# Optimization experiments

Hardware: AMD Instinct MI355X
Metric: run time of the kernel (lower is better)

Reference implementation:

```python
import jax, jax.numpy as jnp
import numpy as np

DT = 0.01


def setup_inputs() -> dict:
    key = jax.random.key(0)
    ks = jax.random.split(key, 16)
    B, T, IN, S, N, OUT, H = 512, 2048, 32, 16, 128, 8, 64
    sc = 0.1
    return {
        "obs": jax.random.normal(ks[0], (B, T, IN), jnp.float32),
        "x0": jnp.zeros((B, S), jnp.float32),
        "A_T": sc * jax.random.normal(ks[1], (S, S), jnp.float32),
        "Bw_T": sc * jax.random.normal(ks[2], (N, S), jnp.float32),
        "By_T": sc * jax.random.normal(ks[3], (IN, S), jnp.float32),
        "Cv_T": sc * jax.random.normal(ks[4], (S, N), jnp.float32),
        "Dvy_T": sc * jax.random.normal(ks[5], (IN, N), jnp.float32),
        "Cu_T": sc * jax.random.normal(ks[6], (S, OUT), jnp.float32),
        "Duw_T": sc * jax.random.normal(ks[7], (N, OUT), jnp.float32),
        "Duy_T": sc * jax.random.normal(ks[8], (IN, OUT), jnp.float32),
        "log_stds": jnp.full((OUT,), -1.6094379124341003, jnp.float32),
        "W1": sc * jax.random.normal(ks[9], (IN, H), jnp.float32),
        "b1": jnp.zeros((H,), jnp.float32),
        "W2": sc * jax.random.normal(ks[10], (H, H), jnp.float32),
        "b2": jnp.zeros((H,), jnp.float32),
        "W3": sc * jax.random.normal(ks[11], (H, 1), jnp.float32),
        "b3": jnp.zeros((1,), jnp.float32),
    }


def reference(obs, x0, A_T, Bw_T, By_T, Cv_T, Dvy_T, Cu_T, Duw_T, Duy_T,
              log_stds, W1, b1, W2, b2, W3, b3):
    B, T, _ = obs.shape

    def xdot(x, y, w=None):
        if w is None:
            w = jnp.tanh(x @ Cv_T + y @ Dvy_T)
        return x @ A_T + w @ Bw_T + y @ By_T

    def step(x, y):
        # y: [B, IN], x: [B, S]
        w = jnp.tanh(x @ Cv_T + y @ Dvy_T)          # [B, N]
        u = x @ Cu_T + w @ Duw_T + y @ Duy_T        # [B, OUT]
        k1 = xdot(x, y, w=w)
        k2 = xdot(x + DT * k1 / 2, y)
        k3 = xdot(x + DT * k2 / 2, y)
        k4 = xdot(x + DT * k3, y)
        x_next = x + DT / 6 * (k1 + 2 * k2 + 2 * k3 + k4)
        return x_next, u

    obs_t = jnp.swapaxes(obs, 0, 1)                 # [T, B, IN]
    x_final, actions_t = jax.lax.scan(step, x0, obs_t)
    actions = jnp.swapaxes(actions_t, 0, 1)         # [B, T, OUT]

    log_stds_rep = jnp.broadcast_to(log_stds, actions.shape[:2] + log_stds.shape)
    outputs = jnp.concatenate((actions, log_stds_rep), axis=2)

    # value baseline MLP over raw observations
    h = jnp.tanh(obs @ W1 + b1)
    h = jnp.tanh(h @ W2 + b2)
    value = (h @ W3 + b3).reshape(-1)               # [B*T]
    return outputs, x_final, value
```

## Files before the change

kernel.cpp:

```cpp
#include <hip/hip_runtime.h>


#define B_SZ  512
#define T_LEN 2048
#define IN_D  32
#define S_D   16
#define N_D   128
#define OUT_D 8
#define H_D   64
#define DT_C  0.01f
#define CHUNK 8
#define NCH   (T_LEN / CHUNK)

typedef unsigned short u16;
typedef unsigned int   u32;
typedef unsigned int uv2 __attribute__((ext_vector_type(2)));

__device__ __forceinline__ float bf2f(u16 u){ return __uint_as_float(((u32)u)<<16); }
__device__ __forceinline__ float lo2f(u32 w){ return __uint_as_float(w<<16); }
__device__ __forceinline__ float hi2f(u32 w){ return __uint_as_float(w & 0xffff0000u); }
__device__ __forceinline__ u16 f2bf(float f){
    u32 u = __float_as_uint(f);
    u32 r = (u + 0x7fffu + ((u>>16)&1u)) >> 16;
    return (u16)r;
}
__device__ __forceinline__ float fast_tanh(float a){
    float e = __builtin_amdgcn_exp2f(a * 2.8853900817779268f);
    float r = __builtin_amdgcn_rcpf(e + 1.0f);
    return fmaf(-2.0f, r, 1.0f);
}
__device__ __forceinline__ u32 getc(const uint4& v, int c){
    return c==0 ? v.x : c==1 ? v.y : c==2 ? v.z : v.w;
}

#define QUAD1 0xB1
#define QUAD2 0x4E
#define QUAD3 0x1B
#define ROR8  0x128
#define HMIR  0x141
#define RMIR  0x140
template<int CTRL>
__device__ __forceinline__ float dppf(float v){
    return __int_as_float(__builtin_amdgcn_update_dpp(
        __float_as_int(v), __float_as_int(v), CTRL, 0xF, 0xF, false));
}
__device__ __forceinline__ float pl16sum(float v){
    uv2 r = __builtin_amdgcn_permlane16_swap(__float_as_uint(v), __float_as_uint(v), false, false);
    return __uint_as_float(r[0]) + __uint_as_float(r[1]);
}
__device__ __forceinline__ float pl32sum(float v){
    uv2 r = __builtin_amdgcn_permlane32_swap(__float_as_uint(v), __float_as_uint(v), false, false);
    return __uint_as_float(r[0]) + __uint_as_float(r[1]);
}

__device__ __forceinline__ int sig4(int d){ return (d&3) ^ ((d&4)?7:0) ^ (d&8); }
__device__ __forceinline__ int sig3(int d){ return (d&3) ^ ((d&4)?7:0); }

template<bool BF16>
__device__ __forceinline__ float ldw(const void* p, int i){
    if (BF16) return bf2f(((const u16*)p)[i]);
    else      return ((const float*)p)[i];
}
template<bool BF16>
__device__ __forceinline__ float yelem(const uint4* yr, int j){
    if (BF16) { u32 w = getc(yr[j>>3], (j>>1)&3); return (j&1) ? hi2f(w) : lo2f(w); }
    else      { return __uint_as_float(getc(yr[j>>2], j&3)); }
}
template<bool BF16>
__device__ __forceinline__ void ldrow(uint4* r, const void* obs, size_t row){
    const uint4* p = (const uint4*)((const char*)obs + row * (size_t)(IN_D * (BF16 ? 2 : 4)));
    #pragma unroll
    for (int q = 0; q < (BF16 ? 4 : 8); ++q) r[q] = p[q];
}
template<bool BF16>
__device__ __forceinline__ void stout(void* out, size_t i, float v){
    if (BF16) ((u16*)out)[i] = f2bf(v);
    else      ((float*)out)[i] = v;
}

template<bool BF16>
__global__ __attribute__((amdgpu_waves_per_eu(1, 1))) __launch_bounds__(128)
void rnn_fused(const void* __restrict__ obs,  const void* __restrict__ x0,
               const void* __restrict__ A_T,  const void* __restrict__ Bw_T,
               const void* __restrict__ By_T, const void* __restrict__ Cv_T,
               const void* __restrict__ Dvy_T,const void* __restrict__ Cu_T,
               const void* __restrict__ Duw_T,const void* __restrict__ Duy_T,
               const void* __restrict__ log_stds,
               const void* __restrict__ W1, const void* __restrict__ b1,
               const void* __restrict__ W2, const void* __restrict__ b2,
               const void* __restrict__ W3, const void* __restrict__ b3,
               void* __restrict__ out)
{
    {
        u32 w0 = *(const u32*)log_stds;
        bool is_bf16 = ((w0 & 0xffffu) == 0xBFCEu);
        if (is_bf16 != BF16) return;
    }

    const int b = blockIdx.x;
    const int t = threadIdx.x;
    const int l = t & 63;
    constexpr int NW = BF16 ? 4 : 8;

    __shared__ __align__(16) float yds[2][CHUNK][160];
    __shared__ __align__(16) float vh[2][64];

    const size_t XF_OFF  = (size_t)B_SZ * T_LEN * 16;
    const size_t VAL_OFF = XF_OFF + (size_t)B_SZ * S_D;

    if (t < 64) {
        const int cx = l & 15;
        const int o8 = l & 7;
        const int n0 = l, n1 = l + 64;

        float Cv0x[16], Cv1x[16], AxCol[16], CuCol[16];
        #pragma unroll
        for (int m = 0; m < 16; ++m) {
            int s = cx ^ m;
            Cv0x[m] = ldw<BF16>(Cv_T, s * N_D + n0);
            Cv1x[m] = ldw<BF16>(Cv_T, s * N_D + n1);
            AxCol[m] = ldw<BF16>(A_T,  s * S_D + cx);
            CuCol[m] = ldw<BF16>(Cu_T, s * OUT_D + o8);
        }
        float Bw0x[16], Bw1x[16];
        #pragma unroll
        for (int d = 0; d < 16; ++d) {
            int s = cx ^ sig4(d);
            Bw0x[d] = ldw<BF16>(Bw_T, n0 * S_D + s);
            Bw1x[d] = ldw<BF16>(Bw_T, n1 * S_D + s);
        }
        float Duw0x[8], Duw1x[8];
        #pragma unroll
        for (int d = 0; d < 8; ++d) {
            int o = o8 ^ sig3(d);
            Duw0x[d] = ldw<BF16>(Duw_T, n0 * OUT_D + o);
            Duw1x[d] = ldw<BF16>(Duw_T, n1 * OUT_D + o);
        }
        const float lsv = ldw<BF16>(log_stds, o8);

        float xb = ldw<BF16>(x0, b * S_D + cx);
        float g[16];
        #pragma unroll
        for (int m = 0; m < 16; ++m) g[m] = ldw<BF16>(x0, b * S_D + (cx ^ m));

        __syncthreads();

        for (int r = 0; r < NCH; ++r) {
            const float (*yb)[160] = yds[r & 1];
            float nD0 = yb[0][l];
            float nD1 = yb[0][64 + l];
            float nXv = yb[0][128 + cx];
            float nUv = yb[0][144 + o8];

            for (int j = 0; j < CHUNK; ++j) {
                const float yD0 = nD0, yD1 = nD1, yXv = nXv, yUv = nUv;
                if (j + 1 < CHUNK) {
                    nD0 = yb[j+1][l];
                    nD1 = yb[j+1][64 + l];
                    nXv = yb[j+1][128 + cx];
                    nUv = yb[j+1][144 + o8];
                }
                const int step = r * CHUNK + j;

                float kacc = 0.f;
                #pragma unroll
                for (int i = 0; i < 4; ++i) {
                    float a0a = 0.f, a0b = 0.f, a0c = 0.f, a0d = 0.f;
                    float a1a = 0.f, a1b = 0.f, a1c = 0.f, a1d = 0.f;
                    #pragma unroll
                    for (int m = 0; m < 4; ++m) {
                        a0a = fmaf(g[m],    Cv0x[m],    a0a);
                        a0b = fmaf(g[m+4],  Cv0x[m+4],  a0b);
                        a0c = fmaf(g[m+8],  Cv0x[m+8],  a0c);
                        a0d = fmaf(g[m+12], Cv0x[m+12], a0d);
                        a1a = fmaf(g[m],    Cv1x[m],    a1a);
                        a1b = fmaf(g[m+4],  Cv1x[m+4],  a1b);
                        a1c = fmaf(g[m+8],  Cv1x[m+8],  a1c);
                        a1d = fmaf(g[m+12], Cv1x[m+12], a1d);
                    }
                    float w0 = fast_tanh(((a0a + a0b) + (a0c + a0d)) + yD0);
                    float w1 = fast_tanh(((a1a + a1b) + (a1c + a1d)) + yD1);

                    float axAa = 0.f, axAb = 0.f, axAc = 0.f, axAd = 0.f;
                    #pragma unroll
                    for (int m = 0; m < 4; ++m) {
                        axAa = fmaf(g[m],    AxCol[m],    axAa);
                        axAb = fmaf(g[m+4],  AxCol[m+4],  axAb);
                        axAc = fmaf(g[m+8],  AxCol[m+8],  axAc);
                        axAd = fmaf(g[m+12], AxCol[m+12], axAd);
                    }
                    float axA = ((axAa + axAb) + (axAc + axAd)) + yXv;

                    float pk[16];
                    #pragma unroll
                    for (int d = 0; d < 16; ++d) pk[d] = fmaf(w1, Bw1x[d], w0 * Bw0x[d]);
                    #pragma unroll
                    for (int d = 0; d < 16; d += 2) pk[d] += dppf<QUAD1>(pk[d+1]);
                    #pragma unroll
                    for (int d = 0; d < 16; d += 4) pk[d] += dppf<QUAD2>(pk[d+2]);
                    pk[0] += dppf<HMIR>(pk[4]);
                    pk[8] += dppf<HMIR>(pk[12]);
                    float krow  = pk[0] + dppf<ROR8>(pk[8]);
                    float kfull = pl32sum(pl16sum(krow)) + axA;

                    if (i == 0) {
                        float axCua = 0.f, axCub = 0.f;
                        #pragma unroll
                        for (int m = 0; m < 8; ++m) {
                            axCua = fmaf(g[m],   CuCol[m],   axCua);
                            axCub = fmaf(g[m+8], CuCol[m+8], axCub);
                        }
                        float pu[8];
                        #pragma unroll
                        for (int d = 0; d < 8; ++d) pu[d] = fmaf(w1, Duw1x[d], w0 * Duw0x[d]);
                        #pragma unroll
                        for (int d = 0; d < 8; d += 2) pu[d] += dppf<QUAD1>(pu[d+1]);
                        pu[0] += dppf<QUAD2>(pu[2]);
                        pu[4] += dppf<QUAD2>(pu[6]);
                        float urow = pu[0] + dppf<HMIR>(pu[4]);
                        urow += dppf<ROR8>(urow);
                        float uo = pl32sum(pl16sum(urow)) + ((axCua + axCub) + yUv);
                        if (l < 16) {
                            size_t ob = ((size_t)b * T_LEN + step) * 16;
                            stout<BF16>(out, ob + l, (l < 8) ? uo : lsv);
                        }
                    }

                    kacc += ((i == 1 || i == 2) ? 2.0f : 1.0f) * kfull;
                    float xnew;
                    if (i == 0 || i == 1) xnew = fmaf(0.5f * DT_C, kfull, xb);
                    else if (i == 2)      xnew = fmaf(DT_C, kfull, xb);
                    else { xb = fmaf(DT_C * (1.0f / 6.0f), kacc, xb); xnew = xb; }

                    g[0]  = xnew;
                    g[1]  = dppf<QUAD1>(g[0]);
                    g[2]  = dppf<QUAD2>(g[0]);
                    g[3]  = dppf<QUAD3>(g[0]);
                    g[7]  = dppf<HMIR>(g[0]);
                    g[6]  = dppf<QUAD1>(g[7]);
                    g[5]  = dppf<QUAD2>(g[7]);
                    g[4]  = dppf<QUAD3>(g[7]);
                    g[8]  = dppf<ROR8>(g[0]);
                    g[9]  = dppf<QUAD1>(g[8]);
                    g[10] = dppf<QUAD2>(g[8]);
                    g[11] = dppf<QUAD3>(g[8]);
                    g[15] = dppf<RMIR>(g[0]);
                    g[14] = dppf<QUAD1>(g[15]);
                    g[13] = dppf<QUAD2>(g[15]);
                    g[12] = dppf<QUAD3>(g[15]);
                }
            }
            __syncthreads();
        }
        if (l < 16) {
            stout<BF16>(out, XF_OFF + (size_t)b * S_D + l, xb);
        }
    } else {
        float Dvy0[32], Dvy1[32];
        #pragma unroll
        for (int j = 0; j < 32; ++j) {
            Dvy0[j] = ldw<BF16>(Dvy_T, j * N_D + l);
            Dvy1[j] = ldw<BF16>(Dvy_T, j * N_D + 64 + l);
        }
        float XC[32];
        #pragma unroll
        for (int j = 0; j < 32; ++j) {
            float v = 0.f;
            if (l >= 16 && l < 32) v = ldw<BF16>(By_T,  j * S_D   + (l & 15));
            if (l >= 48 && l < 56) v = ldw<BF16>(Duy_T, j * OUT_D + (l & 7));
            XC[j] = v;
        }
        float W1c[32], W2c[64];
        #pragma unroll
        for (int j = 0; j < 32; ++j) W1c[j] = ldw<BF16>(W1, j * H_D + l);
        #pragma unroll
        for (int j = 0; j < 64; ++j) W2c[j] = ldw<BF16>(W2, j * H_D + l);
        float b1l = ldw<BF16>(b1, l);
        float b2l = ldw<BF16>(b2, l);
        float w3l = ldw<BF16>(W3, l);
        float b3f = ldw<BF16>(b3, 0);

        auto body = [&](int row, const uint4* yc) {
            float d0a=0.f,d0b=0.f,d1a=0.f,d1b=0.f,xea=0.f,xeb=0.f;
            #pragma unroll
            for (int j = 0; j < 16; ++j) {
                float ya = yelem<BF16>(yc, j), yb2 = yelem<BF16>(yc, j + 16);
                d0a = fmaf(ya,  Dvy0[j],    d0a);
                d0b = fmaf(yb2, Dvy0[j+16], d0b);
                d1a = fmaf(ya,  Dvy1[j],    d1a);
                d1b = fmaf(yb2, Dvy1[j+16], d1b);
                xea = fmaf(ya,  XC[j],      xea);
                xeb = fmaf(yb2, XC[j+16],   xeb);
            }
            float* db = yds[(row / CHUNK) & 1][row % CHUNK];
            db[l]      = d0a + d0b;
            db[64 + l] = d1a + d1b;
            float xev = xea + xeb;
            if (l >= 16 && l < 32) db[128 + (l - 16)] = xev;
            if (l >= 48 && l < 56) db[144 + (l - 48)] = xev;

            float h1a = b1l, h1b = 0.f;
            #pragma unroll
            for (int j = 0; j < 16; ++j) {
                h1a = fmaf(yelem<BF16>(yc, j),      W1c[j],    h1a);
                h1b = fmaf(yelem<BF16>(yc, j + 16), W1c[j+16], h1b);
            }
            float h1 = fast_tanh(h1a + h1b);
            float* vhb = vh[row & 1];
            vhb[l] = h1;
            float h2a = b2l, h2b = 0.f, h2c = 0.f, h2d = 0.f;
            #pragma unroll
            for (int q = 0; q < 16; ++q) {
                float4 v4 = *(const float4*)&vhb[q * 4];
                float* acc = (q & 2) ? ((q & 1) ? &h2d : &h2c)
                                     : ((q & 1) ? &h2b : &h2a);
                *acc = fmaf(v4.x, W2c[q*4+0], *acc);
                *acc = fmaf(v4.y, W2c[q*4+1], *acc);
                *acc = fmaf(v4.z, W2c[q*4+2], *acc);
                *acc = fmaf(v4.w, W2c[q*4+3], *acc);
            }
            float h2 = fast_tanh((h2a + h2b) + (h2c + h2d));
            float v = h2 * w3l;
            v += dppf<QUAD1>(v);
            v += dppf<QUAD2>(v);
            v += dppf<HMIR>(v);
            v += dppf<ROR8>(v);
            v = pl32sum(pl16sum(v));
            if (l == 0) {
                size_t rr = (size_t)b * T_LEN + row;
                stout<BF16>(out, VAL_OFF + rr, v + b3f);
            }
        };

        uint4 yrA[NW], yrB[NW];
        const size_t base = (size_t)b * T_LEN;
        ldrow<BF16>(yrA, obs, base + 0);
        ldrow<BF16>(yrB, obs, base + 1);

        auto produce = [&](int c) {
            for (int jj = 0; jj < CHUNK; jj += 2) {
                int row = c * CHUNK + jj;
                body(row, yrA);
                { int nr = row + 2; if (nr > T_LEN - 1) nr = T_LEN - 1;
                  ldrow<BF16>(yrA, obs, base + nr); }
                body(row + 1, yrB);
                { int nr = row + 3; if (nr > T_LEN - 1) nr = T_LEN - 1;
                  ldrow<BF16>(yrB, obs, base + nr); }
            }
        };

        produce(0);
        __syncthreads();

        for (int r = 0; r < NCH; ++r) {
            if (r < NCH - 1) produce(r + 1);
            __syncthreads();
        }
    }
}

extern "C" void kernel_launch(void* const* d_in, const int* in_sizes, int n_in,
                              void* d_out, int out_size, void* d_ws, size_t ws_size,
                              hipStream_t stream) {
    (void)in_sizes; (void)n_in; (void)out_size; (void)d_ws; (void)ws_size;
    rnn_fused<true><<<dim3(B_SZ), dim3(128), 0, stream>>>(
        d_in[0], d_in[1], d_in[2], d_in[3], d_in[4], d_in[5], d_in[6], d_in[7],
        d_in[8], d_in[9], d_in[10], d_in[11], d_in[12], d_in[13], d_in[14],
        d_in[15], d_in[16], d_out);
    rnn_fused<false><<<dim3(B_SZ), dim3(128), 0, stream>>>(
        d_in[0], d_in[1], d_in[2], d_in[3], d_in[4], d_in[5], d_in[6], d_in[7],
        d_in[8], d_in[9], d_in[10], d_in[11], d_in[12], d_in[13], d_in[14],
        d_in[15], d_in[16], d_out);
}
```

Before: 3.022 ms.

## Offload action output computation from recurrent wave to producer wave via LDS

The serial recurrence wave no longer computes the action output u = x·Cu + w·Duw + y·Duy on each step. It writes x and w to a double-buffered LDS staging area, and the producer wave computes u one chunk later and stores it. This shortens the critical recurrent path and frees registers there, at the cost of extra LDS writes and more work on the producer wave, which could itself become the bottleneck.

```diff
diff --git a/kernel.cpp b/kernel.cpp
--- a/kernel.cpp
+++ b/kernel.cpp
@@ -103,6 +103,8 @@
     constexpr int NW = BF16 ? 4 : 8;
 
     __shared__ __align__(16) float yds[2][CHUNK][160];
+    __shared__ __align__(16) float wlds[2][CHUNK][144];
+    __shared__ __align__(16) float uY[2][CHUNK][8];
     __shared__ __align__(16) float vh[2][64];
 
     const size_t XF_OFF  = (size_t)B_SZ * T_LEN * 16;
@@ -110,17 +112,15 @@
 
     if (t < 64) {
         const int cx = l & 15;
-        const int o8 = l & 7;
         const int n0 = l, n1 = l + 64;
 
-        float Cv0x[16], Cv1x[16], AxCol[16], CuCol[16];
+        float Cv0x[16], Cv1x[16], AxCol[16];
         #pragma unroll
         for (int m = 0; m < 16; ++m) {
             int s = cx ^ m;
             Cv0x[m] = ldw<BF16>(Cv_T, s * N_D + n0);
             Cv1x[m] = ldw<BF16>(Cv_T, s * N_D + n1);
             AxCol[m] = ldw<BF16>(A_T,  s * S_D + cx);
-            CuCol[m] = ldw<BF16>(Cu_T, s * OUT_D + o8);
         }
         float Bw0x[16], Bw1x[16];
         #pragma unroll
@@ -129,14 +129,6 @@
             Bw0x[d] = ldw<BF16>(Bw_T, n0 * S_D + s);
             Bw1x[d] = ldw<BF16>(Bw_T, n1 * S_D + s);
         }
-        float Duw0x[8], Duw1x[8];
-        #pragma unroll
-        for (int d = 0; d < 8; ++d) {
-            int o = o8 ^ sig3(d);
-            Duw0x[d] = ldw<BF16>(Duw_T, n0 * OUT_D + o);
-            Duw1x[d] = ldw<BF16>(Duw_T, n1 * OUT_D + o);
-        }
-        const float lsv = ldw<BF16>(log_stds, o8);
 
         float xb = ldw<BF16>(x0, b * S_D + cx);
         float g[16];
@@ -147,20 +139,18 @@
 
         for (int r = 0; r < NCH; ++r) {
             const float (*yb)[160] = yds[r & 1];
+            float (*wl)[144] = wlds[r & 1];
             float nD0 = yb[0][l];
             float nD1 = yb[0][64 + l];
             float nXv = yb[0][128 + cx];
-            float nUv = yb[0][144 + o8];
 
             for (int j = 0; j < CHUNK; ++j) {
-                const float yD0 = nD0, yD1 = nD1, yXv = nXv, yUv = nUv;
+                const float yD0 = nD0, yD1 = nD1, yXv = nXv;
                 if (j + 1 < CHUNK) {
                     nD0 = yb[j+1][l];
                     nD1 = yb[j+1][64 + l];
                     nXv = yb[j+1][128 + cx];
-                    nUv = yb[j+1][144 + o8];
                 }
-                const int step = r * CHUNK + j;
 
                 float kacc = 0.f;
                 #pragma unroll
@@ -181,6 +171,12 @@
                     float w0 = fast_tanh(((a0a + a0b) + (a0c + a0d)) + yD0);
                     float w1 = fast_tanh(((a1a + a1b) + (a1c + a1d)) + yD1);
 
+                    if (i == 0) {
+                        wl[j][16 + l] = w0;
+                        wl[j][80 + l] = w1;
+                        if (l < 16) wl[j][l] = g[0];
+                    }
+
                     float axAa = 0.f, axAb = 0.f, axAc = 0.f, axAd = 0.f;
                     #pragma unroll
                     for (int m = 0; m < 4; ++m) {
@@ -202,29 +198,6 @@
                     pk[8] += dppf<HMIR>(pk[12]);
                     float krow  = pk[0] + dppf<ROR8>(pk[8]);
                     float kfull = pl32sum(pl16sum(krow)) + axA;
-
-                    if (i == 0) {
-                        float axCua = 0.f, axCub = 0.f;
-                        #pragma unroll
-                        for (int m = 0; m < 8; ++m) {
-                            axCua = fmaf(g[m],   CuCol[m],   axCua);
-                            axCub = fmaf(g[m+8], CuCol[m+8], axCub);
-                        }
-                        float pu[8];
-                        #pragma unroll
-                        for (int d = 0; d < 8; ++d) pu[d] = fmaf(w1, Duw1x[d], w0 * Duw0x[d]);
-                        #pragma unroll
-                        for (int d = 0; d < 8; d += 2) pu[d] += dppf<QUAD1>(pu[d+1]);
-                        pu[0] += dppf<QUAD2>(pu[2]);
-                        pu[4] += dppf<QUAD2>(pu[6]);
-                        float urow = pu[0] + dppf<HMIR>(pu[4]);
-                        urow += dppf<ROR8>(urow);
-                        float uo = pl32sum(pl16sum(urow)) + ((axCua + axCub) + yUv);
-                        if (l < 16) {
-                            size_t ob = ((size_t)b * T_LEN + step) * 16;
-                            stout<BF16>(out, ob + l, (l < 8) ? uo : lsv);
-                        }
-                    }
 
                     kacc += ((i == 1 || i == 2) ? 2.0f : 1.0f) * kfull;
                     float xnew;
@@ -256,6 +229,7 @@
             stout<BF16>(out, XF_OFF + (size_t)b * S_D + l, xb);
         }
     } else {
+        const int o8 = l & 7;
         float Dvy0[32], Dvy1[32];
         #pragma unroll
         for (int j = 0; j < 32; ++j) {
@@ -270,6 +244,15 @@
             if (l >= 48 && l < 56) v = ldw<BF16>(Duy_T, j * OUT_D + (l & 7));
             XC[j] = v;
         }
+        float Duw0u[8], Duw1u[8], Cuu[8];
+        #pragma unroll
+        for (int d = 0; d < 8; ++d) {
+            int o = o8 ^ sig3(d);
+            Duw0u[d] = ldw<BF16>(Duw_T, l * OUT_D + o);
+            Duw1u[d] = ldw<BF16>(Duw_T, (l + 64) * OUT_D + o);
+            Cuu[d]   = (l < 16) ? ldw<BF16>(Cu_T, l * OUT_D + o) : 0.f;
+        }
+        const float lsv = ldw<BF16>(log_stds, o8);
         float W1c[32], W2c[64];
         #pragma unroll
         for (int j = 0; j < 32; ++j) W1c[j] = ldw<BF16>(W1, j * H_D + l);
@@ -292,12 +275,13 @@
                 xea = fmaf(ya,  XC[j],      xea);
                 xeb = fmaf(yb2, XC[j+16],   xeb);
             }
-            float* db = yds[(row / CHUNK) & 1][row % CHUNK];
+            const int par = (row / CHUNK) & 1, jj = row % CHUNK;
+            float* db = yds[par][jj];
             db[l]      = d0a + d0b;
             db[64 + l] = d1a + d1b;
             float xev = xea + xeb;
             if (l >= 16 && l < 32) db[128 + (l - 16)] = xev;
-            if (l >= 48 && l < 56) db[144 + (l - 48)] = xev;
+            if (l >= 48 && l < 56) uY[par][jj][l - 48] = xev;
 
             float h1a = b1l, h1b = 0.f;
             #pragma unroll
@@ -332,6 +316,31 @@
             }
         };
 
+        auto def_u = [&](int q, int rbase) {
+            for (int jj = 0; jj < CHUNK; ++jj) {
+                float xv  = wlds[q][jj][l];
+                float w0v = wlds[q][jj][16 + l];
+                float w1v = wlds[q][jj][80 + l];
+                float pu[8];
+                #pragma unroll
+                for (int d = 0; d < 8; ++d) {
+                    pu[d] = fmaf(w1v, Duw1u[d], w0v * Duw0u[d]);
+                    pu[d] = fmaf(xv, Cuu[d], pu[d]);
+                }
+                #pragma unroll
+                for (int d = 0; d < 8; d += 2) pu[d] += dppf<QUAD1>(pu[d+1]);
+                pu[0] += dppf<QUAD2>(pu[2]);
+                pu[4] += dppf<QUAD2>(pu[6]);
+                float urow = pu[0] + dppf<HMIR>(pu[4]);
+                urow += dppf<ROR8>(urow);
+                float uo = pl32sum(pl16sum(urow)) + uY[q][jj][o8];
+                if (l < 16) {
+                    size_t ob = ((size_t)b * T_LEN + rbase + jj) * 16;
+                    stout<BF16>(out, ob + l, (l < 8) ? uo : lsv);
+                }
+            }
+        };
+
         uint4 yrA[NW], yrB[NW];
         const size_t base = (size_t)b * T_LEN;
         ldrow<BF16>(yrA, obs, base + 0);
@@ -353,9 +362,11 @@
         __syncthreads();
 
         for (int r = 0; r < NCH; ++r) {
+            if (r > 0) def_u((r - 1) & 1, (r - 1) * CHUNK);
             if (r < NCH - 1) produce(r + 1);
             __syncthreads();
         }
+        def_u((NCH - 1) & 1, (NCH - 1) * CHUNK);
     }
 }
 
```

Result: slower. 3.213 ms (+6.3%).

## Pack recurrent matvecs into float2 FMAs and fold A/Cu into butterfly reductions

Applied to the files above, without the earlier changes.

Pairs the two hidden-unit columns and the Bw/Duw rows into float2 vectors so the compiler can emit packed FMA instructions on the serial recurrence path. The x@A and x@Cu products are no longer separate 16-wide dot products. Each lane now adds its own scaled row contribution into the existing DPP/permlane reduction tree, with the y-projection terms pre-divided to compensate for replication across lanes. This cuts per-step FMA count on the latency-bound scan. It changes the floating-point summation order and relies on the replication factors (0.25, 0.125) matching the reduction fan-in exactly.

```diff
diff --git a/kernel.cpp b/kernel.cpp
--- a/kernel.cpp
+++ b/kernel.cpp
@@ -15,6 +15,7 @@
 typedef unsigned short u16;
 typedef unsigned int   u32;
 typedef unsigned int uv2 __attribute__((ext_vector_type(2)));
+typedef float f32x2 __attribute__((ext_vector_type(2)));
 
 __device__ __forceinline__ float bf2f(u16 u){ return __uint_as_float(((u32)u)<<16); }
 __device__ __forceinline__ float lo2f(u32 w){ return __uint_as_float(w<<16); }
@@ -31,6 +32,9 @@
 }
 __device__ __forceinline__ u32 getc(const uint4& v, int c){
     return c==0 ? v.x : c==1 ? v.y : c==2 ? v.z : v.w;
+}
+__device__ __forceinline__ f32x2 fma2(f32x2 a, f32x2 b, f32x2 c){
+    return __builtin_elementwise_fma(a, b, c);
 }
 
 #define QUAD1 0xB1
@@ -113,28 +117,34 @@
         const int o8 = l & 7;
         const int n0 = l, n1 = l + 64;
 
-        float Cv0x[16], Cv1x[16], AxCol[16], CuCol[16];
+        f32x2 Cvp[16];
         #pragma unroll
         for (int m = 0; m < 16; ++m) {
             int s = cx ^ m;
-            Cv0x[m] = ldw<BF16>(Cv_T, s * N_D + n0);
-            Cv1x[m] = ldw<BF16>(Cv_T, s * N_D + n1);
-            AxCol[m] = ldw<BF16>(A_T,  s * S_D + cx);
-            CuCol[m] = ldw<BF16>(Cu_T, s * OUT_D + o8);
-        }
-        float Bw0x[16], Bw1x[16];
-        #pragma unroll
-        for (int d = 0; d < 16; ++d) {
-            int s = cx ^ sig4(d);
-            Bw0x[d] = ldw<BF16>(Bw_T, n0 * S_D + s);
-            Bw1x[d] = ldw<BF16>(Bw_T, n1 * S_D + s);
-        }
-        float Duw0x[8], Duw1x[8];
-        #pragma unroll
-        for (int d = 0; d < 8; ++d) {
-            int o = o8 ^ sig3(d);
-            Duw0x[d] = ldw<BF16>(Duw_T, n0 * OUT_D + o);
-            Duw1x[d] = ldw<BF16>(Duw_T, n1 * OUT_D + o);
+            Cvp[m] = (f32x2){ ldw<BF16>(Cv_T, s * N_D + n0),
+                              ldw<BF16>(Cv_T, s * N_D + n1) };
+        }
+        f32x2 Bw0p[8], Bw1p[8], AxRp[8];
+        #pragma unroll
+        for (int p = 0; p < 8; ++p) {
+            int s0 = cx ^ sig4(2*p), s1 = cx ^ sig4(2*p+1);
+            Bw0p[p] = (f32x2){ ldw<BF16>(Bw_T, n0 * S_D + s0),
+                               ldw<BF16>(Bw_T, n0 * S_D + s1) };
+            Bw1p[p] = (f32x2){ ldw<BF16>(Bw_T, n1 * S_D + s0),
+                               ldw<BF16>(Bw_T, n1 * S_D + s1) };
+            AxRp[p] = (f32x2){ 0.25f * ldw<BF16>(A_T, cx * S_D + s0),
+                               0.25f * ldw<BF16>(A_T, cx * S_D + s1) };
+        }
+        f32x2 Duw0p[4], Duw1p[4], CuRp[4];
+        #pragma unroll
+        for (int p = 0; p < 4; ++p) {
+            int o0 = o8 ^ sig3(2*p), o1 = o8 ^ sig3(2*p+1);
+            Duw0p[p] = (f32x2){ ldw<BF16>(Duw_T, n0 * OUT_D + o0),
+                                ldw<BF16>(Duw_T, n0 * OUT_D + o1) };
+            Duw1p[p] = (f32x2){ ldw<BF16>(Duw_T, n1 * OUT_D + o0),
+                                ldw<BF16>(Duw_T, n1 * OUT_D + o1) };
+            CuRp[p]  = (f32x2){ 0.25f * ldw<BF16>(Cu_T, cx * OUT_D + o0),
+                                0.25f * ldw<BF16>(Cu_T, cx * OUT_D + o1) };
         }
         const float lsv = ldw<BF16>(log_stds, o8);
 
@@ -149,77 +159,78 @@
             const float (*yb)[160] = yds[r & 1];
             float nD0 = yb[0][l];
             float nD1 = yb[0][64 + l];
-            float nXv = yb[0][128 + cx];
-            float nUv = yb[0][144 + o8];
+            float nXq = yb[0][128 + cx];
+            float nUq = yb[0][144 + o8];
 
             for (int j = 0; j < CHUNK; ++j) {
-                const float yD0 = nD0, yD1 = nD1, yXv = nXv, yUv = nUv;
+                const float yD0 = nD0, yD1 = nD1, yXq = nXq, yUq = nUq;
                 if (j + 1 < CHUNK) {
                     nD0 = yb[j+1][l];
                     nD1 = yb[j+1][64 + l];
-                    nXv = yb[j+1][128 + cx];
-                    nUv = yb[j+1][144 + o8];
+                    nXq = yb[j+1][128 + cx];
+                    nUq = yb[j+1][144 + o8];
                 }
                 const int step = r * CHUNK + j;
 
                 float kacc = 0.f;
                 #pragma unroll
                 for (int i = 0; i < 4; ++i) {
-                    float a0a = 0.f, a0b = 0.f, a0c = 0.f, a0d = 0.f;
-                    float a1a = 0.f, a1b = 0.f, a1c = 0.f, a1d = 0.f;
+                    f32x2 ac0 = (f32x2){yD0, yD1};
+                    f32x2 ac1 = (f32x2){0.f, 0.f};
+                    f32x2 ac2 = (f32x2){0.f, 0.f};
+                    f32x2 ac3 = (f32x2){0.f, 0.f};
                     #pragma unroll
                     for (int m = 0; m < 4; ++m) {
-                        a0a = fmaf(g[m],    Cv0x[m],    a0a);
-                        a0b = fmaf(g[m+4],  Cv0x[m+4],  a0b);
-                        a0c = fmaf(g[m+8],  Cv0x[m+8],  a0c);
-                        a0d = fmaf(g[m+12], Cv0x[m+12], a0d);
-                        a1a = fmaf(g[m],    Cv1x[m],    a1a);
-                        a1b = fmaf(g[m+4],  Cv1x[m+4],  a1b);
-                        a1c = fmaf(g[m+8],  Cv1x[m+8],  a1c);
-                        a1d = fmaf(g[m+12], Cv1x[m+12], a1d);
+                        ac0 = fma2((f32x2){g[m],    g[m]},    Cvp[m],    ac0);
+                        ac1 = fma2((f32x2){g[m+4],  g[m+4]},  Cvp[m+4],  ac1);
+                        ac2 = fma2((f32x2){g[m+8],  g[m+8]},  Cvp[m+8],  ac2);
+                        ac3 = fma2((f32x2){g[m+12], g[m+12]}, Cvp[m+12], ac3);
                     }
-                    float w0 = fast_tanh(((a0a + a0b) + (a0c + a0d)) + yD0);
-                    float w1 = fast_tanh(((a1a + a1b) + (a1c + a1d)) + yD1);
-
-                    float axAa = 0.f, axAb = 0.f, axAc = 0.f, axAd = 0.f;
+                    f32x2 a01 = (ac0 + ac1) + (ac2 + ac3);
+                    float w0 = fast_tanh(a01.x);
+                    float w1 = fast_tanh(a01.y);
+
+                    f32x2 w0s = (f32x2){w0, w0};
+                    f32x2 w1s = (f32x2){w1, w1};
+                    f32x2 g0s = (f32x2){g[0], g[0]};
+                    f32x2 pk2[8];
                     #pragma unroll
-                    for (int m = 0; m < 4; ++m) {
-                        axAa = fmaf(g[m],    AxCol[m],    axAa);
-                        axAb = fmaf(g[m+4],  AxCol[m+4],  axAb);
-                        axAc = fmaf(g[m+8],  AxCol[m+8],  axAc);
-                        axAd = fmaf(g[m+12], AxCol[m+12], axAd);
+                    for (int p = 0; p < 8; ++p) {
+                        pk2[p] = fma2(w1s, Bw1p[p], w0s * Bw0p[p]);
+                        pk2[p] = fma2(g0s, AxRp[p], pk2[p]);
                     }
-                    float axA = ((axAa + axAb) + (axAc + axAd)) + yXv;
-
-                    float pk[16];
+                    pk2[0].x += yXq;
+
+                    float qa[8];
                     #pragma unroll
-                    for (int d = 0; d < 16; ++d) pk[d] = fmaf(w1, Bw1x[d], w0 * Bw0x[d]);
+                    for (int p = 0; p < 8; ++p)
+                        qa[p] = pk2[p].x + dppf<QUAD1>(pk2[p].y);
+                    float qb[4];
                     #pragma unroll
-                    for (int d = 0; d < 16; d += 2) pk[d] += dppf<QUAD1>(pk[d+1]);
-                    #pragma unroll
-                    for (int d = 0; d < 16; d += 4) pk[d] += dppf<QUAD2>(pk[d+2]);
-                    pk[0] += dppf<HMIR>(pk[4]);
-                    pk[8] += dppf<HMIR>(pk[12]);
-                    float krow  = pk[0] + dppf<ROR8>(pk[8]);
-                    float kfull = pl32sum(pl16sum(krow)) + axA;
+                    for (int jj = 0; jj < 4; ++jj)
+                        qb[jj] = qa[2*jj] + dppf<QUAD2>(qa[2*jj+1]);
+                    float qc0 = qb[0] + dppf<HMIR>(qb[1]);
+                    float qc1 = qb[2] + dppf<HMIR>(qb[3]);
+                    float krow  = qc0 + dppf<ROR8>(qc1);
+                    float kfull = pl32sum(pl16sum(krow));
 
                     if (i == 0) {
-                        float axCua = 0.f, axCub = 0.f;
+                        f32x2 pu2[4];
                         #pragma unroll
-                        for (int m = 0; m < 8; ++m) {
-                            axCua = fmaf(g[m],   CuCol[m],   axCua);
-                            axCub = fmaf(g[m+8], CuCol[m+8], axCub);
+                        for (int p = 0; p < 4; ++p) {
+                            pu2[p] = fma2(w1s, Duw1p[p], w0s * Duw0p[p]);
+                            pu2[p] = fma2(g0s, CuRp[p], pu2[p]);
                         }
-                        float pu[8];
+                        pu2[0].x += yUq;
+                        float ua[4];
                         #pragma unroll
-                        for (int d = 0; d < 8; ++d) pu[d] = fmaf(w1, Duw1x[d], w0 * Duw0x[d]);
-                        #pragma unroll
-                        for (int d = 0; d < 8; d += 2) pu[d] += dppf<QUAD1>(pu[d+1]);
-                        pu[0] += dppf<QUAD2>(pu[2]);
-                        pu[4] += dppf<QUAD2>(pu[6]);
-                        float urow = pu[0] + dppf<HMIR>(pu[4]);
+                        for (int p = 0; p < 4; ++p)
+                            ua[p] = pu2[p].x + dppf<QUAD1>(pu2[p].y);
+                        float ub0 = ua[0] + dppf<QUAD2>(ua[1]);
+                        float ub1 = ua[2] + dppf<QUAD2>(ua[3]);
+                        float urow = ub0 + dppf<HMIR>(ub1);
                         urow += dppf<ROR8>(urow);
-                        float uo = pl32sum(pl16sum(urow)) + ((axCua + axCub) + yUv);
+                        float uo = pl32sum(pl16sum(urow));
                         if (l < 16) {
                             size_t ob = ((size_t)b * T_LEN + step) * 16;
                             stout<BF16>(out, ob + l, (l < 8) ? uo : lsv);
@@ -296,8 +307,8 @@
             db[l]      = d0a + d0b;
             db[64 + l] = d1a + d1b;
             float xev = xea + xeb;
-            if (l >= 16 && l < 32) db[128 + (l - 16)] = xev;
-            if (l >= 48 && l < 56) db[144 + (l - 48)] = xev;
+            if (l >= 16 && l < 32) db[128 + (l - 16)] = xev * 0.25f;
+            if (l >= 48 && l < 56) db[144 + (l - 48)] = xev * 0.125f;
 
             float h1a = b1l, h1b = 0.f;
             #pragma unroll
```

Measured after the change: 2.871 ms. 5.0% less time.
